# Kernel tuning notes

Measured on AMD Instinct MI355X. Metric: run time of the kernel, lower is better.

Reference implementation:

```python
import jax, jax.numpy as jnp
import numpy as np

B, N, C, K = 8, 2048, 512, 1


def setup_inputs() -> dict:
    key = jax.random.key(0)
    ks = jax.random.split(key, 10)
    s = 1.0 / np.sqrt(C)
    f32 = jnp.float32
    return {
        "x": jax.random.normal(ks[0], (B, N, C), f32),
        "neighbors": jax.random.randint(ks[1], (N, K), 0, N),
        "Wq": jax.random.normal(ks[2], (C, C), f32) * s,
        "bq": jnp.zeros((C,), f32),
        "Wk": jax.random.normal(ks[3], (C, C), f32) * s,
        "bk": jnp.zeros((C,), f32),
        "Wv": jax.random.normal(ks[4], (C, C), f32) * s,
        "bv": jnp.zeros((C,), f32),
        "rel_bias": jnp.zeros((K, K), f32),  # nn.Parameter(torch.zeros(k,k))
        "Wo": jax.random.normal(ks[5], (C, C), f32) * s,
        "bo": jnp.zeros((C,), f32),
    }


def reference(x, neighbors, Wq, bq, Wk, bk, Wv, bv, rel_bias, Wo, bo):
    # torch Linear: y = x @ W.T + b
    Q = jnp.einsum("bnc,dc->bnd", x, Wq) + bq
    Kt = jnp.einsum("bnc,dc->bnd", x, Wk) + bk
    V = jnp.einsum("bnc,dc->bnd", x, Wv) + bv

    nbr = neighbors[:, 0]  # [N], the single neighbor of each position (k==1)
    Kn = Kt[:, nbr, :]     # [B,N,C] gathered keys
    Vn = V[:, nbr, :]      # [B,N,C] gathered values (V_neighbors viewed as [B,N,k*C])

    # per-position score q_i . k_{nbr_i} + bias scalar
    s = jnp.einsum("bnc,bnc->bn", Q, Kn) + rel_bias[0, 0]

    # dense NxN score matrix, zeros elsewhere (faithful: softmax includes the zeros)
    scores = jnp.zeros((B, N, N), x.dtype).at[:, jnp.arange(N), nbr].set(s)
    probs = jax.nn.softmax(scores / jnp.asarray(np.sqrt(C), x.dtype), axis=-1)

    out = jnp.einsum("bnm,bmc->bnc", probs, Vn)
    return jnp.einsum("bnc,dc->bnd", out, Wo) + bo
```

## Files before the change

kernel.cpp:

```cpp
#include <hip/hip_runtime.h>
#include <hip/hip_bf16.h>
#include <math.h>

namespace {
constexpr int kB = 8;
constexpr int kN = 2048;
constexpr int kC = 512;
constexpr int kR = kB * kN;
constexpr int kNC = 2 * kC;
constexpr float kInvSqrtC = 0.044194173824159216f;

typedef __attribute__((ext_vector_type(8))) short short8;
typedef __attribute__((ext_vector_type(4))) short short4b;
typedef __attribute__((ext_vector_type(4))) float f32x4;
typedef unsigned short ushort;
}

static __device__ __forceinline__ float bf2f(ushort u) {
  union { unsigned int i; float f; } v; v.i = (unsigned int)u << 16; return v.f;
}
static __device__ __forceinline__ ushort f2bf(float f) {
  __hip_bfloat16 h = __float2bfloat16(f);
  union { __hip_bfloat16 h; ushort u; } cv; cv.h = h; return cv.u;
}

#define GLOAD16(G, L) __builtin_amdgcn_global_load_lds( \
    (const __attribute__((address_space(1))) unsigned int*)(G), \
    (__attribute__((address_space(3))) unsigned int*)(L), 16, 0, 0)

__global__ __launch_bounds__(256) void castw_kernel(
    const float* __restrict__ Wq, const float* __restrict__ Wk,
    const float* __restrict__ Wv, const float* __restrict__ Wo,
    ushort* __restrict__ WqT, ushort* __restrict__ WkT,
    ushort* __restrict__ WvT, ushort* __restrict__ Woh,
    const int* __restrict__ nbr, int* __restrict__ cnt) {
  const int z = blockIdx.z;
  const int t = threadIdx.x;
  if (z == 4) {
    if (blockIdx.x || blockIdx.y) return;
    __shared__ int h[kN];
#pragma unroll
    for (int i = 0; i < 8; i++) h[t + i * 256] = 0;
    __syncthreads();
#pragma unroll
    for (int i = 0; i < 8; i++) atomicAdd(&h[nbr[t + i * 256]], 1);
    __syncthreads();
#pragma unroll
    for (int i = 0; i < 8; i++) cnt[t + i * 256] = h[t + i * 256];
    return;
  }
  const int d0 = blockIdx.x * 64, c0 = blockIdx.y * 64;
  if (z == 3) {
#pragma unroll
    for (int i = 0; i < 4; i++) {
      const int row = i * 16 + (t >> 4), col4 = (t & 15) * 4;
      const float4 v = *reinterpret_cast<const float4*>(&Wo[(d0 + row) * kC + c0 + col4]);
      short4b o;
      o[0] = (short)f2bf(v.x); o[1] = (short)f2bf(v.y);
      o[2] = (short)f2bf(v.z); o[3] = (short)f2bf(v.w);
      *reinterpret_cast<short4b*>(&Woh[(d0 + row) * kC + c0 + col4]) = o;
    }
    return;
  }
  __shared__ float ld[64][65];
  const float* S = (z == 0) ? Wq : ((z == 1) ? Wk : Wv);
  ushort* T = (z == 0) ? WqT : ((z == 1) ? WkT : WvT);
#pragma unroll
  for (int i = 0; i < 4; i++) {
    const int dl = i * 16 + (t >> 4), cl4 = (t & 15) * 4;
    const float4 v = *reinterpret_cast<const float4*>(&S[(d0 + dl) * kC + c0 + cl4]);
    ld[dl][cl4 + 0] = v.x; ld[dl][cl4 + 1] = v.y;
    ld[dl][cl4 + 2] = v.z; ld[dl][cl4 + 3] = v.w;
  }
  __syncthreads();
#pragma unroll
  for (int i = 0; i < 4; i++) {
    const int cl = i * 16 + (t >> 4), dl4 = (t & 15) * 4;
    short4b o;
#pragma unroll
    for (int q = 0; q < 4; q++) o[q] = (short)f2bf(ld[dl4 + q][cl]);
    *reinterpret_cast<short4b*>(&T[(size_t)(c0 + cl) * kC + d0 + dl4]) = o;
  }
}

__global__ __launch_bounds__(256) void fold_kernel(
    const ushort* __restrict__ WqT, const ushort* __restrict__ WkT,
    const ushort* __restrict__ Woh, const ushort* __restrict__ WvT,
    ushort* __restrict__ Bh,
    const float* __restrict__ bq, const float* __restrict__ bk, const float* __restrict__ bv,
    float* __restrict__ biascat, float* __restrict__ vbq, float* __restrict__ bqbk) {
  const int t = threadIdx.x, lane = t & 63, w = t >> 6;
  const int z = blockIdx.z;
  if (z == 2) {
    const int fid = blockIdx.y * 8 + blockIdx.x;
    const int gw = fid * 4 + w;
    for (int rr = gw; rr < 1536; rr += 256) {
      const ushort* rowp; const float* vec;
      if (rr < 512)       { rowp = &WqT[(size_t)rr * kC];          vec = bk; }
      else if (rr < 1024) { rowp = &WkT[(size_t)(rr - 512) * kC];  vec = bq; }
      else                { rowp = &Woh[(size_t)(rr - 1024) * kC]; vec = bv; }
      const short8 u = *reinterpret_cast<const short8*>(&rowp[lane * 8]);
      const float4 v0 = *reinterpret_cast<const float4*>(&vec[lane * 8]);
      const float4 v1 = *reinterpret_cast<const float4*>(&vec[lane * 8 + 4]);
      float a = bf2f((ushort)u[0]) * v0.x + bf2f((ushort)u[1]) * v0.y +
                bf2f((ushort)u[2]) * v0.z + bf2f((ushort)u[3]) * v0.w +
                bf2f((ushort)u[4]) * v1.x + bf2f((ushort)u[5]) * v1.y +
                bf2f((ushort)u[6]) * v1.z + bf2f((ushort)u[7]) * v1.w;
#pragma unroll
      for (int off = 32; off; off >>= 1) a += __shfl_xor(a, off);
      if (lane == 0) {
        if (rr < 512) biascat[rr] = a;
        else if (rr < 1024) vbq[rr - 512] = a;
        else biascat[rr - 512] = a;
      }
    }
    if (gw == 0) {
      const float4 q0 = *reinterpret_cast<const float4*>(&bq[lane * 8]);
      const float4 q1 = *reinterpret_cast<const float4*>(&bq[lane * 8 + 4]);
      const float4 k0 = *reinterpret_cast<const float4*>(&bk[lane * 8]);
      const float4 k1 = *reinterpret_cast<const float4*>(&bk[lane * 8 + 4]);
      float s = q0.x * k0.x + q0.y * k0.y + q0.z * k0.z + q0.w * k0.w +
                q1.x * k1.x + q1.y * k1.y + q1.z * k1.z + q1.w * k1.w;
#pragma unroll
      for (int off = 32; off; off >>= 1) s += __shfl_xor(s, off);
      if (lane == 0) bqbk[0] = s;
    }
    return;
  }
  __shared__ ushort lA[64 * 64];
  __shared__ ushort lB[64 * 64];
  const ushort* Ap = z ? Woh : WqT;
  const ushort* Bp = z ? WvT : WkT;
  const int r0 = blockIdx.y * 64, c0 = blockIdx.x * 64;
  const int wr = (w >> 1) * 32, wc = (w & 1) * 32;
  const int srow = t >> 3, scol = (t & 7) * 8;
  f32x4 acc[2][2] = {};
  for (int k0 = 0; k0 < kC; k0 += 64) {
#pragma unroll
    for (int it = 0; it < 2; it++) {
      GLOAD16(&Ap[(size_t)(r0 + it * 32 + srow) * kC + k0 + scol], &lA[(it * 32 + srow) * 64 + scol]);
      GLOAD16(&Bp[(size_t)(c0 + it * 32 + srow) * kC + k0 + scol], &lB[(it * 32 + srow) * 64 + scol]);
    }
    __syncthreads();
#pragma unroll
    for (int kk = 0; kk < 2; kk++) {
      const int ko = kk * 32 + (lane >> 4) * 8;
      short8 af[2], bfr[2];
#pragma unroll
      for (int i = 0; i < 2; i++)
        af[i] = *reinterpret_cast<const short8*>(&lA[(wr + i * 16 + (lane & 15)) * 64 + ko]);
#pragma unroll
      for (int j = 0; j < 2; j++)
        bfr[j] = *reinterpret_cast<const short8*>(&lB[(wc + j * 16 + (lane & 15)) * 64 + ko]);
#pragma unroll
      for (int i = 0; i < 2; i++)
#pragma unroll
        for (int j = 0; j < 2; j++)
          acc[i][j] = __builtin_amdgcn_mfma_f32_16x16x32_bf16(af[i], bfr[j], acc[i][j], 0, 0, 0);
    }
    __syncthreads();
  }
#pragma unroll
  for (int j = 0; j < 2; j++) {
    const int col = c0 + wc + j * 16 + (lane & 15);
#pragma unroll
    for (int i = 0; i < 2; i++) {
      const int rbase = r0 + wr + i * 16 + (lane >> 4) * 4;
#pragma unroll
      for (int q = 0; q < 4; q++)
        Bh[(size_t)(z * kC + rbase + q) * kC + col] = f2bf(acc[i][j][q]);
    }
  }
}

__global__ __launch_bounds__(256) void castg_kernel(
    const float* __restrict__ x, const float* __restrict__ vbq,
    ushort* __restrict__ xh, float* __restrict__ g) {
  const int wid = threadIdx.x >> 6, lane = threadIdx.x & 63;
  const int r = blockIdx.x * 4 + wid;
  const float4 a = *reinterpret_cast<const float4*>(&x[(size_t)r * kC + lane * 8]);
  const float4 b = *reinterpret_cast<const float4*>(&x[(size_t)r * kC + lane * 8 + 4]);
  short8 o;
  o[0] = (short)f2bf(a.x); o[1] = (short)f2bf(a.y);
  o[2] = (short)f2bf(a.z); o[3] = (short)f2bf(a.w);
  o[4] = (short)f2bf(b.x); o[5] = (short)f2bf(b.y);
  o[6] = (short)f2bf(b.z); o[7] = (short)f2bf(b.w);
  *reinterpret_cast<short8*>(&xh[(size_t)r * kC + lane * 8]) = o;
  const float4 v0 = *reinterpret_cast<const float4*>(&vbq[lane * 8]);
  const float4 v1 = *reinterpret_cast<const float4*>(&vbq[lane * 8 + 4]);
  float acc = a.x * v0.x + a.y * v0.y + a.z * v0.z + a.w * v0.w +
              b.x * v1.x + b.y * v1.y + b.z * v1.z + b.w * v1.w;
#pragma unroll
  for (int off = 32; off; off >>= 1) acc += __shfl_xor(acc, off);
  if (lane == 0) g[r] = acc;
}

__global__ __launch_bounds__(256) void mm_kernel(
    const ushort* __restrict__ xh, const ushort* __restrict__ Bh,
    const float* __restrict__ biascat, ushort* __restrict__ obuf) {
  __shared__ ushort lA[2][128 * 64];
  __shared__ ushort lB[2][128 * 64];
  const int id = blockIdx.x;
  const int orig = (id & 7) * 128 + (id >> 3);
  const int r0 = (orig >> 3) * 128;
  const int c0 = (orig & 7) * 128;
  const int t = threadIdx.x;
  const int lane = t & 63, w = t >> 6;
  const int wr = (w >> 1) * 64, wc = (w & 1) * 64;
  const int srow = t >> 3, scol = (t & 7) * 8;
  f32x4 acc[4][4] = {};

  auto stage = [&](int buf, int k0) {
#pragma unroll
    for (int it = 0; it < 4; it++) {
      GLOAD16(&xh[(size_t)(r0 + it * 32 + srow) * kC + k0 + scol],
              &lA[buf][(it * 32 + srow) * 64 + scol]);
      GLOAD16(&Bh[(size_t)(c0 + it * 32 + srow) * kC + k0 + scol],
              &lB[buf][(it * 32 + srow) * 64 + scol]);
    }
  };

  stage(0, 0);
  __syncthreads();
  int cur = 0;
#pragma unroll
  for (int ts = 0; ts < 8; ++ts) {
    if (ts < 7) stage(cur ^ 1, (ts + 1) * 64);
#pragma unroll
    for (int kk = 0; kk < 2; kk++) {
      const int ko = kk * 32 + (lane >> 4) * 8;
      short8 af[4], bfr[4];
#pragma unroll
      for (int i = 0; i < 4; i++)
        af[i] = *reinterpret_cast<const short8*>(&lA[cur][(wr + i * 16 + (lane & 15)) * 64 + ko]);
#pragma unroll
      for (int j = 0; j < 4; j++)
        bfr[j] = *reinterpret_cast<const short8*>(&lB[cur][(wc + j * 16 + (lane & 15)) * 64 + ko]);
      __builtin_amdgcn_s_setprio(1);
#pragma unroll
      for (int i = 0; i < 4; i++)
#pragma unroll
        for (int j = 0; j < 4; j++)
          acc[i][j] = __builtin_amdgcn_mfma_f32_16x16x32_bf16(af[i], bfr[j], acc[i][j], 0, 0, 0);
      __builtin_amdgcn_s_setprio(0);
    }
    __syncthreads();
    cur ^= 1;
  }
#pragma unroll
  for (int j = 0; j < 4; j++) {
    const int col = c0 + wc + j * 16 + (lane & 15);
    const float bias = biascat[col];
#pragma unroll
    for (int i = 0; i < 4; i++) {
      const int rbase = r0 + wr + i * 16 + (lane >> 4) * 4;
#pragma unroll
      for (int q = 0; q < 4; q++)
        obuf[(size_t)(rbase + q) * kNC + col] = f2bf(acc[i][j][q] + bias);
    }
  }
}

__global__ __launch_bounds__(256) void svo_part_kernel(
    const ushort* __restrict__ obuf, const int* __restrict__ cnt, float* __restrict__ part) {
  const int d = blockIdx.x * 256 + threadIdx.x;
  const int jc = blockIdx.y;
  const int b = blockIdx.z;
  float a = 0.f;
  for (int j = jc * 64; j < jc * 64 + 64; j++) {
    const int cj = cnt[j];
    if (cj) a += (float)cj * bf2f(obuf[(size_t)(b * kN + j) * kNC + kC + d]);
  }
  part[(size_t)(b * 32 + jc) * kC + d] = a;
}

__global__ __launch_bounds__(256) void svo_reduce_kernel(
    const float* __restrict__ part, float* __restrict__ svo) {
  const int d = blockIdx.x * 256 + threadIdx.x;
  const int b = blockIdx.y;
  float a = 0.f;
#pragma unroll
  for (int jc = 0; jc < 32; jc++) a += part[(size_t)(b * 32 + jc) * kC + d];
  svo[b * kC + d] = a;
}

__global__ __launch_bounds__(256) void final_kernel(
    const ushort* __restrict__ xh, const ushort* __restrict__ obuf,
    const float* __restrict__ svo, const float* __restrict__ g, const int* __restrict__ nbr,
    const float* __restrict__ bqbk, const float* __restrict__ rb, const float* __restrict__ bo,
    float* __restrict__ out) {
  const int wid = threadIdx.x >> 6, lane = threadIdx.x & 63;
  const int rg = blockIdx.x * 4 + wid;
  const int b = rg >> 11, n = rg & (kN - 1);
  const int j = nbr[n];
  const int j2 = nbr[j];
  const short8 xv = *reinterpret_cast<const short8*>(&xh[(size_t)rg * kC + lane * 8]);
  const short8 wv = *reinterpret_cast<const short8*>(&obuf[(size_t)(b * kN + j) * kNC + lane * 8]);
  float a = 0.f;
#pragma unroll
  for (int q = 0; q < 8; q++) a += bf2f((ushort)xv[q]) * bf2f((ushort)wv[q]);
#pragma unroll
  for (int off = 32; off; off >>= 1) a += __shfl_xor(a, off);
  const float s = a + g[b * kN + j] + bqbk[0] + rb[0];
  const float tt = s * kInvSqrtC;
  const float e = expf(tt);
  const float inv = 1.0f / (e + (float)(kN - 1));
  const float coef = (e - 1.0f) * inv;
  const short8 vv = *reinterpret_cast<const short8*>(&obuf[(size_t)(b * kN + j2) * kNC + kC + lane * 8]);
  const float4 s0 = *reinterpret_cast<const float4*>(&svo[b * kC + lane * 8]);
  const float4 s1 = *reinterpret_cast<const float4*>(&svo[b * kC + lane * 8 + 4]);
  const float4 b0 = *reinterpret_cast<const float4*>(&bo[lane * 8]);
  const float4 b1 = *reinterpret_cast<const float4*>(&bo[lane * 8 + 4]);
  float4 r0, r1;
  r0.x = s0.x * inv + bf2f((ushort)vv[0]) * coef + b0.x;
  r0.y = s0.y * inv + bf2f((ushort)vv[1]) * coef + b0.y;
  r0.z = s0.z * inv + bf2f((ushort)vv[2]) * coef + b0.z;
  r0.w = s0.w * inv + bf2f((ushort)vv[3]) * coef + b0.w;
  r1.x = s1.x * inv + bf2f((ushort)vv[4]) * coef + b1.x;
  r1.y = s1.y * inv + bf2f((ushort)vv[5]) * coef + b1.y;
  r1.z = s1.z * inv + bf2f((ushort)vv[6]) * coef + b1.z;
  r1.w = s1.w * inv + bf2f((ushort)vv[7]) * coef + b1.w;
  *reinterpret_cast<float4*>(&out[(size_t)rg * kC + lane * 8]) = r0;
  *reinterpret_cast<float4*>(&out[(size_t)rg * kC + lane * 8 + 4]) = r1;
}

extern "C" void kernel_launch(void* const* d_in, const int* in_sizes, int n_in,
                              void* d_out, int out_size, void* d_ws, size_t ws_size,
                              hipStream_t stream) {
  const float* x  = (const float*)d_in[0];
  const int* nbr  = (const int*)d_in[1];
  const float* Wq = (const float*)d_in[2];
  const float* bq = (const float*)d_in[3];
  const float* Wk = (const float*)d_in[4];
  const float* bk = (const float*)d_in[5];
  const float* Wv = (const float*)d_in[6];
  const float* bv = (const float*)d_in[7];
  const float* rb = (const float*)d_in[8];
  const float* Wo = (const float*)d_in[9];
  const float* bo = (const float*)d_in[10];
  float* out = (float*)d_out;

  char* ws = (char*)d_ws;
  size_t off = 0;
  auto alloc = [&](size_t bytes) -> void* {
    void* p = ws + off;
    off = (off + bytes + 255) & ~(size_t)255;
    return p;
  };
  ushort* xh    = (ushort*)alloc((size_t)kR * kC * 2);
  ushort* Bh    = (ushort*)alloc((size_t)kNC * kC * 2);
  ushort* obuf  = (ushort*)alloc((size_t)kR * kNC * 2);
  ushort* WqT   = (ushort*)alloc((size_t)kC * kC * 2);
  ushort* WkT   = (ushort*)alloc((size_t)kC * kC * 2);
  ushort* WvT   = (ushort*)alloc((size_t)kC * kC * 2);
  ushort* Woh   = (ushort*)alloc((size_t)kC * kC * 2);
  float* biascat = (float*)alloc(kNC * 4);
  float* vbq    = (float*)alloc(kC * 4);
  float* bqbk   = (float*)alloc(4);
  int*   cnt    = (int*)alloc(kN * 4);
  float* g      = (float*)alloc((size_t)kR * 4);
  float* svo    = (float*)alloc((size_t)kB * kC * 4);
  float* part   = (float*)alloc((size_t)kB * 32 * kC * 4);
  (void)ws_size; (void)n_in; (void)in_sizes; (void)out_size;

  castw_kernel<<<dim3(8, 8, 5), 256, 0, stream>>>(Wq, Wk, Wv, Wo, WqT, WkT, WvT, Woh, nbr, cnt);
  fold_kernel<<<dim3(8, 8, 3), 256, 0, stream>>>(WqT, WkT, Woh, WvT, Bh, bq, bk, bv, biascat, vbq, bqbk);
  castg_kernel<<<kR / 4, 256, 0, stream>>>(x, vbq, xh, g);
  mm_kernel<<<1024, 256, 0, stream>>>(xh, Bh, biascat, obuf);
  svo_part_kernel<<<dim3(2, 32, kB), 256, 0, stream>>>(obuf, cnt, part);
  svo_reduce_kernel<<<dim3(2, kB), 256, 0, stream>>>(part, svo);
  final_kernel<<<kR / 4, 256, 0, stream>>>(xh, obuf, svo, g, nbr, bqbk, rb, bo, out);
}
```

Baseline: 84.66 us.

## Deepen GEMM prefetch with vmcnt waits and fuse svo reduction via last-block atomic

The bf16 GEMM now keeps two K-stages in flight. It issues loads for stage ts+2 after a raw s_barrier and waits with an explicit s_waitcnt vmcnt instead of full __syncthreads, so global-to-LDS copies overlap more with MFMA work. Separately, the svo partial-sum and reduce kernels are merged: each block bumps an atomic counter, and the last block per (batch, half) does the 32-way reduction. This saves one kernel launch but adds threadfences, an atomic, and a counter reset in the cast kernel.

```diff
diff --git a/kernel.cpp b/kernel.cpp
--- a/kernel.cpp
+++ b/kernel.cpp
@@ -33,7 +33,7 @@
     const float* __restrict__ Wv, const float* __restrict__ Wo,
     ushort* __restrict__ WqT, ushort* __restrict__ WkT,
     ushort* __restrict__ WvT, ushort* __restrict__ Woh,
-    const int* __restrict__ nbr, int* __restrict__ cnt) {
+    const int* __restrict__ nbr, int* __restrict__ cnt, int* __restrict__ done) {
   const int z = blockIdx.z;
   const int t = threadIdx.x;
   if (z == 4) {
@@ -47,6 +47,7 @@
     __syncthreads();
 #pragma unroll
     for (int i = 0; i < 8; i++) cnt[t + i * 256] = h[t + i * 256];
+    if (t < 16) done[t] = 0;
     return;
   }
   const int d0 = blockIdx.x * 64, c0 = blockIdx.y * 64;
@@ -221,11 +222,14 @@
   };
 
   stage(0, 0);
-  __syncthreads();
-  int cur = 0;
+  stage(1, 64);
 #pragma unroll
   for (int ts = 0; ts < 8; ++ts) {
-    if (ts < 7) stage(cur ^ 1, (ts + 1) * 64);
+    const int cur = ts & 1;
+    if (ts < 7) { asm volatile("s_waitcnt vmcnt(8)" ::: "memory"); }
+    else        { asm volatile("s_waitcnt vmcnt(0)" ::: "memory"); }
+    __builtin_amdgcn_s_barrier();
+    __builtin_amdgcn_sched_barrier(0);
 #pragma unroll
     for (int kk = 0; kk < 2; kk++) {
       const int ko = kk * 32 + (lane >> 4) * 8;
@@ -244,8 +248,10 @@
           acc[i][j] = __builtin_amdgcn_mfma_f32_16x16x32_bf16(af[i], bfr[j], acc[i][j], 0, 0, 0);
       __builtin_amdgcn_s_setprio(0);
     }
-    __syncthreads();
-    cur ^= 1;
+    __builtin_amdgcn_sched_barrier(0);
+    __builtin_amdgcn_s_barrier();
+    __builtin_amdgcn_sched_barrier(0);
+    if (ts < 6) stage(cur, (ts + 2) * 64);
   }
 #pragma unroll
   for (int j = 0; j < 4; j++) {
@@ -261,8 +267,9 @@
   }
 }
 
-__global__ __launch_bounds__(256) void svo_part_kernel(
-    const ushort* __restrict__ obuf, const int* __restrict__ cnt, float* __restrict__ part) {
+__global__ __launch_bounds__(256) void svo_kernel(
+    const ushort* __restrict__ obuf, const int* __restrict__ cnt,
+    float* __restrict__ part, float* __restrict__ svo, int* __restrict__ done) {
   const int d = blockIdx.x * 256 + threadIdx.x;
   const int jc = blockIdx.y;
   const int b = blockIdx.z;
@@ -272,16 +279,18 @@
     if (cj) a += (float)cj * bf2f(obuf[(size_t)(b * kN + j) * kNC + kC + d]);
   }
   part[(size_t)(b * 32 + jc) * kC + d] = a;
-}
-
-__global__ __launch_bounds__(256) void svo_reduce_kernel(
-    const float* __restrict__ part, float* __restrict__ svo) {
-  const int d = blockIdx.x * 256 + threadIdx.x;
-  const int b = blockIdx.y;
-  float a = 0.f;
-#pragma unroll
-  for (int jc = 0; jc < 32; jc++) a += part[(size_t)(b * 32 + jc) * kC + d];
-  svo[b * kC + d] = a;
+  __threadfence();
+  __syncthreads();
+  __shared__ int oldv;
+  if (threadIdx.x == 0) oldv = atomicAdd(&done[b * 2 + blockIdx.x], 1);
+  __syncthreads();
+  if (oldv == 31) {
+    __threadfence();
+    float s = 0.f;
+#pragma unroll
+    for (int jc2 = 0; jc2 < 32; jc2++) s += part[(size_t)(b * 32 + jc2) * kC + d];
+    svo[b * kC + d] = s;
+  }
 }
 
 __global__ __launch_bounds__(256) void final_kernel(
@@ -358,16 +367,16 @@
   float* vbq    = (float*)alloc(kC * 4);
   float* bqbk   = (float*)alloc(4);
   int*   cnt    = (int*)alloc(kN * 4);
+  int*   done   = (int*)alloc(16 * 4);
   float* g      = (float*)alloc((size_t)kR * 4);
   float* svo    = (float*)alloc((size_t)kB * kC * 4);
   float* part   = (float*)alloc((size_t)kB * 32 * kC * 4);
   (void)ws_size; (void)n_in; (void)in_sizes; (void)out_size;
 
-  castw_kernel<<<dim3(8, 8, 5), 256, 0, stream>>>(Wq, Wk, Wv, Wo, WqT, WkT, WvT, Woh, nbr, cnt);
+  castw_kernel<<<dim3(8, 8, 5), 256, 0, stream>>>(Wq, Wk, Wv, Wo, WqT, WkT, WvT, Woh, nbr, cnt, done);
   fold_kernel<<<dim3(8, 8, 3), 256, 0, stream>>>(WqT, WkT, Woh, WvT, Bh, bq, bk, bv, biascat, vbq, bqbk);
   castg_kernel<<<kR / 4, 256, 0, stream>>>(x, vbq, xh, g);
   mm_kernel<<<1024, 256, 0, stream>>>(xh, Bh, biascat, obuf);
-  svo_part_kernel<<<dim3(2, 32, kB), 256, 0, stream>>>(obuf, cnt, part);
-  svo_reduce_kernel<<<dim3(2, kB), 256, 0, stream>>>(part, svo);
+  svo_kernel<<<dim3(2, 32, kB), 256, 0, stream>>>(obuf, cnt, part, svo, done);
   final_kernel<<<kR / 4, 256, 0, stream>>>(xh, obuf, svo, g, nbr, bqbk, rb, bo, out);
 }
```

Result: slower. 119.8 us (+41.6%).

## Deepen GEMM prefetch with vmcnt waits and vectorize svo partial reduction

Applied to the files above, without the earlier changes.

The GEMM mainloop now issues two stages of global-to-LDS loads up front. It replaces __syncthreads with an explicit s_waitcnt vmcnt plus s_barrier, so the next tile's loads stay in flight while MFMAs run on the current one. The svo partial-sum kernel is rewritten to load 8 bf16 per lane as vectors, with four waves splitting rows and reducing through LDS, which doubles the partition count. The gain is more memory/compute overlap and wider loads. The risk is fragile hand-tuned vmcnt counts and a larger partial buffer to reduce.

```diff
diff --git a/kernel.cpp b/kernel.cpp
--- a/kernel.cpp
+++ b/kernel.cpp
@@ -221,11 +221,14 @@
   };
 
   stage(0, 0);
-  __syncthreads();
-  int cur = 0;
+  stage(1, 64);
 #pragma unroll
   for (int ts = 0; ts < 8; ++ts) {
-    if (ts < 7) stage(cur ^ 1, (ts + 1) * 64);
+    const int cur = ts & 1;
+    if (ts < 7) { asm volatile("s_waitcnt vmcnt(8)" ::: "memory"); }
+    else        { asm volatile("s_waitcnt vmcnt(0)" ::: "memory"); }
+    __builtin_amdgcn_s_barrier();
+    __builtin_amdgcn_sched_barrier(0);
 #pragma unroll
     for (int kk = 0; kk < 2; kk++) {
       const int ko = kk * 32 + (lane >> 4) * 8;
@@ -244,8 +247,10 @@
           acc[i][j] = __builtin_amdgcn_mfma_f32_16x16x32_bf16(af[i], bfr[j], acc[i][j], 0, 0, 0);
       __builtin_amdgcn_s_setprio(0);
     }
-    __syncthreads();
-    cur ^= 1;
+    __builtin_amdgcn_sched_barrier(0);
+    __builtin_amdgcn_s_barrier();
+    __builtin_amdgcn_sched_barrier(0);
+    if (ts < 6) stage(cur, (ts + 2) * 64);
   }
 #pragma unroll
   for (int j = 0; j < 4; j++) {
@@ -263,15 +268,33 @@
 
 __global__ __launch_bounds__(256) void svo_part_kernel(
     const ushort* __restrict__ obuf, const int* __restrict__ cnt, float* __restrict__ part) {
-  const int d = blockIdx.x * 256 + threadIdx.x;
-  const int jc = blockIdx.y;
-  const int b = blockIdx.z;
-  float a = 0.f;
-  for (int j = jc * 64; j < jc * 64 + 64; j++) {
+  const int jc = blockIdx.x;
+  const int b = blockIdx.y;
+  const int w = threadIdx.x >> 6, lane = threadIdx.x & 63;
+  const int d0 = lane * 8;
+  float acc[8] = {};
+#pragma unroll
+  for (int i = 0; i < 8; i++) {
+    const int j = jc * 32 + i * 4 + w;
     const int cj = cnt[j];
-    if (cj) a += (float)cj * bf2f(obuf[(size_t)(b * kN + j) * kNC + kC + d]);
-  }
-  part[(size_t)(b * 32 + jc) * kC + d] = a;
+    if (cj) {
+      const short8 v = *reinterpret_cast<const short8*>(&obuf[(size_t)(b * kN + j) * kNC + kC + d0]);
+      const float c = (float)cj;
+#pragma unroll
+      for (int q = 0; q < 8; q++) acc[q] += c * bf2f((ushort)v[q]);
+    }
+  }
+  __shared__ float red[4][kC];
+#pragma unroll
+  for (int q = 0; q < 8; q++) red[w][d0 + q] = acc[q];
+  __syncthreads();
+  if (w == 0) {
+#pragma unroll
+    for (int q = 0; q < 8; q++) {
+      const int d = d0 + q;
+      part[(size_t)(b * 64 + jc) * kC + d] = red[0][d] + red[1][d] + red[2][d] + red[3][d];
+    }
+  }
 }
 
 __global__ __launch_bounds__(256) void svo_reduce_kernel(
@@ -280,7 +303,7 @@
   const int b = blockIdx.y;
   float a = 0.f;
 #pragma unroll
-  for (int jc = 0; jc < 32; jc++) a += part[(size_t)(b * 32 + jc) * kC + d];
+  for (int jc = 0; jc < 64; jc++) a += part[(size_t)(b * 64 + jc) * kC + d];
   svo[b * kC + d] = a;
 }
 
@@ -360,14 +383,14 @@
   int*   cnt    = (int*)alloc(kN * 4);
   float* g      = (float*)alloc((size_t)kR * 4);
   float* svo    = (float*)alloc((size_t)kB * kC * 4);
-  float* part   = (float*)alloc((size_t)kB * 32 * kC * 4);
+  float* part   = (float*)alloc((size_t)kB * 64 * kC * 4);
   (void)ws_size; (void)n_in; (void)in_sizes; (void)out_size;
 
   castw_kernel<<<dim3(8, 8, 5), 256, 0, stream>>>(Wq, Wk, Wv, Wo, WqT, WkT, WvT, Woh, nbr, cnt);
   fold_kernel<<<dim3(8, 8, 3), 256, 0, stream>>>(WqT, WkT, Woh, WvT, Bh, bq, bk, bv, biascat, vbq, bqbk);
   castg_kernel<<<kR / 4, 256, 0, stream>>>(x, vbq, xh, g);
   mm_kernel<<<1024, 256, 0, stream>>>(xh, Bh, biascat, obuf);
-  svo_part_kernel<<<dim3(2, 32, kB), 256, 0, stream>>>(obuf, cnt, part);
+  svo_part_kernel<<<dim3(64, kB), 256, 0, stream>>>(obuf, cnt, part);
   svo_reduce_kernel<<<dim3(2, kB), 256, 0, stream>>>(part, svo);
   final_kernel<<<kR / 4, 256, 0, stream>>>(xh, obuf, svo, g, nbr, bqbk, rb, bo, out);
 }
```

Result: slower. 88.02 us (+4.0%).
